# Performance work log

Hardware: AMD Instinct MI355X
Metric: run time of the kernel (lower is better)

Reference implementation:

```python
import jax, jax.numpy as jnp
import numpy as np

B, TAPE, N, F = 128, 100000, 50000, 32

def setup_inputs() -> dict:
    key = jax.random.key(0)
    k1, k2, k3, k4 = jax.random.split(key, 4)
    tape = jax.random.normal(k1, (B, TAPE), dtype=jnp.float32)
    input_indices = jax.random.randint(k2, (N, F), 0, TAPE)
    # He init scaled by fan-in, padding slots (index==0) zeroed as in __init__
    weights = jax.random.normal(k3, (N, F), dtype=jnp.float32) * jnp.sqrt(2.0 / F)
    weights = jnp.where(input_indices == 0, 0.0, weights)
    bias = jnp.zeros((N,), dtype=jnp.float32)
    output_indices = jnp.arange(N)
    act_type = jax.random.randint(k4, (N,), 0, 2)
    return {"tape": tape, "weights": weights, "bias": bias,
            "input_indices": input_indices, "output_indices": output_indices,
            "act_type": act_type}

def reference(tape, weights, bias, input_indices, output_indices, act_type):
    # gather padded fan-in inputs: [B, N, F]
    gathered = tape[:, input_indices]
    # weighted sum over fan-in + bias: [B, N]
    x = jnp.einsum('bnf,nf->bn', gathered, weights) + bias
    # per-activation-type apply (two activation groups: relu / tanh)
    x = jnp.where(act_type == 0, jax.nn.relu(x), jnp.tanh(x))
    # scatter results back into tape
    return tape.at[:, output_indices].set(x)
```

## Files before the change

### kernel.cpp

```cpp
#include <hip/hip_runtime.h>
#include <cmath>

#define TAPE_SZ 100000
#define N_SZ    50000
#define F_SZ    32
#define B_SZ    128
#define NB      16

static __device__ __forceinline__ unsigned short f32_to_bf16(float f) {
    unsigned int u = __float_as_uint(f);
    u = (u + 0x7fffu + ((u >> 16) & 1u)) >> 16;
    return (unsigned short)u;
}

__global__ __launch_bounds__(256) void transpose_tape(const float* __restrict__ in,
                                                      unsigned short* __restrict__ outT,
                                                      float* __restrict__ out) {
    __shared__ float tile[32][129];
    const int x0 = blockIdx.x * 32;
    const int tx = threadIdx.x;
    const int ty = threadIdx.y;

    const bool tail = (x0 + tx >= N_SZ);
    #pragma unroll
    for (int yy = ty; yy < B_SZ; yy += 8) {
        const float v = in[(size_t)yy * TAPE_SZ + x0 + tx];
        tile[tx][yy] = v;
        if (tail) out[(size_t)yy * TAPE_SZ + x0 + tx] = v;
    }
    __syncthreads();

    const int tid = ty * 32 + tx;
    const int oct = tid & 15;
    const int xl0 = tid >> 4;
    #pragma unroll
    for (int xx = xl0; xx < 32; xx += 16) {
        const float* src = &tile[xx][oct * 8];
        union { unsigned short u[8]; uint4 q; } pk;
        #pragma unroll
        for (int k = 0; k < 8; ++k)
            pk.u[k] = f32_to_bf16(src[k]);
        *(uint4*)(outT + (size_t)(x0 + xx) * B_SZ + oct * 8) = pk.q;
    }
}

__global__ __launch_bounds__(256) void gather_mm(const unsigned short* __restrict__ tapeT,
                                                 const float* __restrict__ weights,
                                                 const float* __restrict__ bias,
                                                 const int*   __restrict__ in_idx,
                                                 const int*   __restrict__ out_idx,
                                                 const int*   __restrict__ act_type,
                                                 float* __restrict__ out) {
    __shared__ int   s_idx[NB][33];
    __shared__ float s_w[NB][33];
    __shared__ float s_bias[NB];
    __shared__ int   s_act[NB];
    __shared__ int   s_oidx[NB];
    __shared__ float s_x[NB][132];

    const int tid = threadIdx.y * 16 + threadIdx.x;
    const int n0  = blockIdx.x * NB;

    #pragma unroll
    for (int t = tid; t < NB * 32; t += 256) {
        const int n = t >> 5, f = t & 31;
        s_idx[n][f] = in_idx[(size_t)n0 * 32 + t];
        s_w[n][f]   = weights[(size_t)n0 * 32 + t];
    }
    if (tid < NB) {
        s_bias[tid] = bias[n0 + tid];
        s_act[tid]  = act_type[n0 + tid];
        s_oidx[tid] = out_idx[n0 + tid];
    }
    __syncthreads();

    const int nl = threadIdx.y;
    const int bx = threadIdx.x;
    float a0 = 0.f, a1 = 0.f, a2 = 0.f, a3 = 0.f, a4 = 0.f, a5 = 0.f, a6 = 0.f, a7 = 0.f;

    #pragma unroll
    for (int fo = 0; fo < 32; fo += 8) {
        int   i8[8]; float w8[8];
        #pragma unroll
        for (int j = 0; j < 8; ++j) { i8[j] = s_idx[nl][fo + j]; w8[j] = s_w[nl][fo + j]; }
        uint4 q8[8];
        #pragma unroll
        for (int j = 0; j < 8; ++j)
            q8[j] = *(const uint4*)(tapeT + (size_t)i8[j] * B_SZ + bx * 8);
        #pragma unroll
        for (int j = 0; j < 8; ++j) {
            const float w = w8[j];
            a0 = fmaf(__uint_as_float(q8[j].x << 16),         w, a0);
            a1 = fmaf(__uint_as_float(q8[j].x & 0xffff0000u), w, a1);
            a2 = fmaf(__uint_as_float(q8[j].y << 16),         w, a2);
            a3 = fmaf(__uint_as_float(q8[j].y & 0xffff0000u), w, a3);
            a4 = fmaf(__uint_as_float(q8[j].z << 16),         w, a4);
            a5 = fmaf(__uint_as_float(q8[j].z & 0xffff0000u), w, a5);
            a6 = fmaf(__uint_as_float(q8[j].w << 16),         w, a6);
            a7 = fmaf(__uint_as_float(q8[j].w & 0xffff0000u), w, a7);
        }
    }

    const float bz = s_bias[nl];
    a0 += bz; a1 += bz; a2 += bz; a3 += bz; a4 += bz; a5 += bz; a6 += bz; a7 += bz;
    if (s_act[nl] == 0) {
        a0 = fmaxf(a0, 0.f); a1 = fmaxf(a1, 0.f); a2 = fmaxf(a2, 0.f); a3 = fmaxf(a3, 0.f);
        a4 = fmaxf(a4, 0.f); a5 = fmaxf(a5, 0.f); a6 = fmaxf(a6, 0.f); a7 = fmaxf(a7, 0.f);
    } else {
        a0 = tanhf(a0); a1 = tanhf(a1); a2 = tanhf(a2); a3 = tanhf(a3);
        a4 = tanhf(a4); a5 = tanhf(a5); a6 = tanhf(a6); a7 = tanhf(a7);
    }
    *(float4*)(&s_x[nl][bx * 8])     = make_float4(a0, a1, a2, a3);
    *(float4*)(&s_x[nl][bx * 8 + 4]) = make_float4(a4, a5, a6, a7);
    __syncthreads();

    const int j    = tid & 15;
    const int brow = tid >> 4;
    const int oc   = s_oidx[j];
    #pragma unroll
    for (int k = 0; k < 8; ++k) {
        const int b = brow + k * 16;
        out[(size_t)b * TAPE_SZ + oc] = s_x[j][b];
    }
}

__global__ __launch_bounds__(128) void gather_fallback(const float* __restrict__ tape,
                                                       const float* __restrict__ weights,
                                                       const float* __restrict__ bias,
                                                       const int*   __restrict__ in_idx,
                                                       const int*   __restrict__ out_idx,
                                                       const int*   __restrict__ act_type,
                                                       float* __restrict__ out) {
    const int n = blockIdx.x;
    const int b = threadIdx.x;
    float acc = 0.f;
    for (int f = 0; f < F_SZ; ++f) {
        acc += tape[(size_t)b * TAPE_SZ + in_idx[(size_t)n * F_SZ + f]] *
               weights[(size_t)n * F_SZ + f];
    }
    acc += bias[n];
    acc = (act_type[n] == 0) ? fmaxf(acc, 0.f) : tanhf(acc);
    out[(size_t)b * TAPE_SZ + out_idx[n]] = acc;
}

__global__ __launch_bounds__(256) void copy_tail_fb(const float* __restrict__ tape,
                                                    float* __restrict__ out) {
    const int n4 = (TAPE_SZ - N_SZ) / 4;
    int i = blockIdx.x * blockDim.x + threadIdx.x;
    int b = blockIdx.y;
    if (i < n4) {
        const float4* src = (const float4*)(tape + (size_t)b * TAPE_SZ + N_SZ);
        float4*       dst = (float4*)(out  + (size_t)b * TAPE_SZ + N_SZ);
        dst[i] = src[i];
    }
}

extern "C" void kernel_launch(void* const* d_in, const int* in_sizes, int n_in,
                              void* d_out, int out_size, void* d_ws, size_t ws_size,
                              hipStream_t stream) {
    const float* tape    = (const float*)d_in[0];
    const float* weights = (const float*)d_in[1];
    const float* bias    = (const float*)d_in[2];
    const int*   in_idx  = (const int*)d_in[3];
    const int*   out_idx = (const int*)d_in[4];
    const int*   act     = (const int*)d_in[5];
    float*       out     = (float*)d_out;

    const size_t need = (size_t)TAPE_SZ * B_SZ * sizeof(unsigned short);
    if (ws_size >= need) {
        unsigned short* tapeT = (unsigned short*)d_ws;
        transpose_tape<<<dim3(TAPE_SZ / 32), dim3(32, 8), 0, stream>>>(tape, tapeT, out);
        gather_mm<<<dim3(N_SZ / NB), dim3(16, 16), 0, stream>>>(
            tapeT, weights, bias, in_idx, out_idx, act, out);
    } else {
        copy_tail_fb<<<dim3(((TAPE_SZ - N_SZ) / 4 + 255) / 256, B_SZ), 256, 0, stream>>>(tape, out);
        gather_fallback<<<dim3(N_SZ), 128, 0, stream>>>(
            tape, weights, bias, in_idx, out_idx, act, out);
    }
}
```

Baseline: 172.8 us.

## Move tail copy into gather kernel blocks and vectorize scatter stores

The transpose kernel no longer writes the untouched tail of the tape to the output. Extra blocks appended to the gather kernel now copy that tail with float4 loads and stores, overlapping the copy with the gather work. The scatter writes each row's four consecutive output columns as one float4 when the output indices are contiguous and 4-aligned, with a scalar fallback otherwise. The extra tail blocks share the grid with gather blocks and may compete for bandwidth.

```diff
diff --git a/kernel.cpp b/kernel.cpp
--- a/kernel.cpp
+++ b/kernel.cpp
@@ -6,6 +6,9 @@
 #define F_SZ    32
 #define B_SZ    128
 #define NB      16
+#define NGATHER 3125
+#define NTAIL   512
+#define TAIL_F4 1600000
 
 static __device__ __forceinline__ unsigned short f32_to_bf16(float f) {
     unsigned int u = __float_as_uint(f);
@@ -14,20 +17,15 @@
 }
 
 __global__ __launch_bounds__(256) void transpose_tape(const float* __restrict__ in,
-                                                      unsigned short* __restrict__ outT,
-                                                      float* __restrict__ out) {
+                                                      unsigned short* __restrict__ outT) {
     __shared__ float tile[32][129];
     const int x0 = blockIdx.x * 32;
     const int tx = threadIdx.x;
     const int ty = threadIdx.y;
 
-    const bool tail = (x0 + tx >= N_SZ);
-    #pragma unroll
-    for (int yy = ty; yy < B_SZ; yy += 8) {
-        const float v = in[(size_t)yy * TAPE_SZ + x0 + tx];
-        tile[tx][yy] = v;
-        if (tail) out[(size_t)yy * TAPE_SZ + x0 + tx] = v;
-    }
+    #pragma unroll
+    for (int yy = ty; yy < B_SZ; yy += 8)
+        tile[tx][yy] = in[(size_t)yy * TAPE_SZ + x0 + tx];
     __syncthreads();
 
     const int tid = ty * 32 + tx;
@@ -50,6 +48,7 @@
                                                  const int*   __restrict__ in_idx,
                                                  const int*   __restrict__ out_idx,
                                                  const int*   __restrict__ act_type,
+                                                 const float* __restrict__ tape,
                                                  float* __restrict__ out) {
     __shared__ int   s_idx[NB][33];
     __shared__ float s_w[NB][33];
@@ -58,8 +57,22 @@
     __shared__ int   s_oidx[NB];
     __shared__ float s_x[NB][132];
 
-    const int tid = threadIdx.y * 16 + threadIdx.x;
-    const int n0  = blockIdx.x * NB;
+    const int tid = threadIdx.x;
+
+    if (blockIdx.x >= NGATHER) {
+        const float4* src = (const float4*)tape;
+        float4*       dst = (float4*)out;
+        const int stride = NTAIL * 256;
+        for (int i = (blockIdx.x - NGATHER) * 256 + tid; i < TAIL_F4; i += stride) {
+            const int b = i / 12500;
+            const int j = i - b * 12500;
+            const int off = b * (TAPE_SZ / 4) + (N_SZ / 4) + j;
+            dst[off] = src[off];
+        }
+        return;
+    }
+
+    const int n0 = blockIdx.x * NB;
 
     #pragma unroll
     for (int t = tid; t < NB * 32; t += 256) {
@@ -74,8 +87,8 @@
     }
     __syncthreads();
 
-    const int nl = threadIdx.y;
-    const int bx = threadIdx.x;
+    const int nl = tid >> 4;
+    const int bx = tid & 15;
     float a0 = 0.f, a1 = 0.f, a2 = 0.f, a3 = 0.f, a4 = 0.f, a5 = 0.f, a6 = 0.f, a7 = 0.f;
 
     #pragma unroll
@@ -110,17 +123,32 @@
         a0 = tanhf(a0); a1 = tanhf(a1); a2 = tanhf(a2); a3 = tanhf(a3);
         a4 = tanhf(a4); a5 = tanhf(a5); a6 = tanhf(a6); a7 = tanhf(a7);
     }
-    *(float4*)(&s_x[nl][bx * 8])     = make_float4(a0, a1, a2, a3);
-    *(float4*)(&s_x[nl][bx * 8 + 4]) = make_float4(a4, a5, a6, a7);
+    {
+        const int b8 = bx * 8;
+        s_x[nl][b8 + 0] = a0; s_x[nl][b8 + 1] = a1; s_x[nl][b8 + 2] = a2; s_x[nl][b8 + 3] = a3;
+        s_x[nl][b8 + 4] = a4; s_x[nl][b8 + 5] = a5; s_x[nl][b8 + 6] = a6; s_x[nl][b8 + 7] = a7;
+    }
     __syncthreads();
 
-    const int j    = tid & 15;
-    const int brow = tid >> 4;
-    const int oc   = s_oidx[j];
-    #pragma unroll
-    for (int k = 0; k < 8; ++k) {
-        const int b = brow + k * 16;
-        out[(size_t)b * TAPE_SZ + oc] = s_x[j][b];
+    const int g  = tid >> 6;
+    const int b0 = tid & 63;
+    const int oc0 = s_oidx[g * 4];
+    const bool consec = (s_oidx[g * 4 + 1] == oc0 + 1) &&
+                        (s_oidx[g * 4 + 2] == oc0 + 2) &&
+                        (s_oidx[g * 4 + 3] == oc0 + 3) && ((oc0 & 3) == 0);
+    #pragma unroll
+    for (int rep = 0; rep < 2; ++rep) {
+        const int b = b0 + rep * 64;
+        const float4 v = make_float4(s_x[g * 4 + 0][b], s_x[g * 4 + 1][b],
+                                     s_x[g * 4 + 2][b], s_x[g * 4 + 3][b]);
+        if (consec) {
+            *(float4*)(out + (size_t)b * TAPE_SZ + oc0) = v;
+        } else {
+            out[(size_t)b * TAPE_SZ + s_oidx[g * 4 + 0]] = v.x;
+            out[(size_t)b * TAPE_SZ + s_oidx[g * 4 + 1]] = v.y;
+            out[(size_t)b * TAPE_SZ + s_oidx[g * 4 + 2]] = v.z;
+            out[(size_t)b * TAPE_SZ + s_oidx[g * 4 + 3]] = v.w;
+        }
     }
 }
 
@@ -169,9 +197,9 @@
     const size_t need = (size_t)TAPE_SZ * B_SZ * sizeof(unsigned short);
     if (ws_size >= need) {
         unsigned short* tapeT = (unsigned short*)d_ws;
-        transpose_tape<<<dim3(TAPE_SZ / 32), dim3(32, 8), 0, stream>>>(tape, tapeT, out);
-        gather_mm<<<dim3(N_SZ / NB), dim3(16, 16), 0, stream>>>(
-            tapeT, weights, bias, in_idx, out_idx, act, out);
+        transpose_tape<<<dim3(TAPE_SZ / 32), dim3(32, 8), 0, stream>>>(tape, tapeT);
+        gather_mm<<<dim3(NGATHER + NTAIL), dim3(256), 0, stream>>>(
+            tapeT, weights, bias, in_idx, out_idx, act, tape, out);
     } else {
         copy_tail_fb<<<dim3(((TAPE_SZ - N_SZ) / 4 + 255) / 256, B_SZ), 256, 0, stream>>>(tape, out);
         gather_fallback<<<dim3(N_SZ), 128, 0, stream>>>(
```

Result: no change. 170.6 us (-1.2%).
